# Kernel tuning notes

Measured on AMD Instinct MI355X. Metric: run time of the kernel, lower is better.

## Reference

```python
import jax, jax.numpy as jnp
import numpy as np

B, S, D, H = 4, 2048, 1024, 1024  # batch, seq, input_dim, hidden_dim

def setup_inputs() -> dict:
    key = jax.random.key(0)
    k1, k2, k3, k4, k5 = jax.random.split(key, 5)
    scale1 = 1.0 / np.sqrt(D)
    scale2 = 1.0 / np.sqrt(H)
    return {
        "x": jax.random.normal(k1, (B, S, D), dtype=jnp.float32),
        "W1": jax.random.uniform(k2, (D, 3 * H), jnp.float32, -scale1, scale1),
        "b1": jax.random.uniform(k3, (3 * H,), jnp.float32, -scale1, scale1),
        "W2": jax.random.uniform(k4, (H, H), jnp.float32, -scale2, scale2),
        "b2": jax.random.uniform(k5, (H,), jnp.float32, -scale2, scale2),
    }

def reference(x, W1, b1, W2, b2):
    qkv = jnp.einsum('bsd,dh->bsh', x, W1) + b1          # [B,S,3H]
    q, k, v = jnp.split(qkv, 3, axis=-1)                  # each [B,S,H]
    scale = (2.0 * D) ** -0.5                             # faithful: (input_dim*2)^-0.5
    scores = jnp.einsum('bse,bSe->bsS', q, k) * scale     # [B,S,S]
    att = jax.nn.softmax(scores, axis=-1)
    ctx = jnp.einsum('bsS,bSe->bse', att, v)              # [B,S,H]
    out = jnp.einsum('bsh,hk->bsk', ctx, W2) + b2
    return out
```

## Files before the change

kernel.cpp:

```cpp
#include <hip/hip_runtime.h>
#include <hip/hip_bf16.h>
#include <stdint.h>

#define B_  4
#define S_  2048
#define D_  1024
#define H_  1024
#define BS_ (B_*S_)
#define N3H (3*H_)

typedef __bf16 bf16x8 __attribute__((ext_vector_type(8)));
typedef float  f32x4  __attribute__((ext_vector_type(4)));
typedef unsigned short u16x8 __attribute__((ext_vector_type(8)));

__device__ __forceinline__ unsigned short f2bf(float x) {
    unsigned u = __float_as_uint(x);
    return (unsigned short)((u + 0x7FFFu + ((u >> 16) & 1u)) >> 16);
}
__device__ __forceinline__ float bf2f(unsigned short h) {
    return __uint_as_float(((unsigned)h) << 16);
}

__device__ __forceinline__ void gload_lds16(const void* g, void* l) {
    __builtin_amdgcn_global_load_lds(
        (const __attribute__((address_space(1))) void*)g,
        (__attribute__((address_space(3))) void*)l, 16, 0, 0);
}

#define BAR __builtin_amdgcn_s_barrier()
#define DS_FENCE do { asm volatile("s_waitcnt lgkmcnt(0)" ::: "memory"); \
                      __builtin_amdgcn_sched_barrier(0); } while (0)

template<int EPI>
__global__ __launch_bounds__(256, 3) void gemm3b(
    const unsigned short* __restrict__ A,
    const unsigned short* __restrict__ Bm,
    int NXt, int NYt, int N, int K,
    long long sAz, long long sBz, long long sOz,
    void* __restrict__ out0, void* __restrict__ out1, void* __restrict__ out2,
    const float* __restrict__ bias, float scale)
{
    __shared__ __align__(16) char lds[3 * 16384];

    const int nt_g = (int)gridDim.x;
    const int bid = (int)blockIdx.x;
    const int C = nt_g >> 3;
    const int c = bid >> 3;
    const int xcd = bid & 7;
    const int qq = c >> 2;
    const int txl = qq % NXt;
    const int rest = (c & 3) + 4 * (qq / NXt);
    const int tile = xcd * C + rest * NXt + txl;
    const int tx = tile % NXt;
    const int rest2 = tile / NXt;
    const int ty = rest2 % NYt;
    const int tz = rest2 / NYt;

    const unsigned short* Ab = A  + (long long)tz * sAz;
    const unsigned short* Bb = Bm + (long long)tz * sBz;
    const int rowBase = ty * 128;
    const int colBase = tx * 128;
    const int tid = threadIdx.x;
    const int w = tid >> 6, l = tid & 63;
    const int wr = w >> 1, wc = w & 1;
    const int fr = l & 15, fq = l >> 4;

    int sr[2], scl[2];
#pragma unroll
    for (int j = 0; j < 2; j++) {
        int o  = j * 4096 + tid * 16;
        int st = o >> 10;
        int wi = o & 1023;
        wi ^= ((wi >> 9) & 1) << 5;
        sr[j]  = st * 16 + (wi >> 6);
        scl[j] = (wi & 63) >> 1;
    }

    auto STAGE_A = [&](char* buf, int t) {
        const unsigned short* base = Ab + (long long)rowBase * K + t * 32;
#pragma unroll
        for (int j = 0; j < 2; j++)
            gload_lds16(base + (long long)sr[j] * K + scl[j],
                        buf + j * 4096 + w * 1024);
    };
    auto STAGE_B = [&](char* buf, int t) {
        const unsigned short* base = Bb + (long long)colBase * K + t * 32;
#pragma unroll
        for (int j = 0; j < 2; j++)
            gload_lds16(base + (long long)sr[j] * K + scl[j],
                        buf + 8192 + j * 4096 + w * 1024);
    };

    const int abase = (fr * 64 + fq * 16) ^ ((fr & 8) << 2);

    f32x4 acc[4][4];
#pragma unroll
    for (int m = 0; m < 4; m++)
#pragma unroll
        for (int n = 0; n < 4; n++) acc[m][n] = (f32x4){0.f, 0.f, 0.f, 0.f};

    const int NT = K >> 5;

    STAGE_A(lds, 0); STAGE_B(lds, 0);
    STAGE_A(lds + 16384, 1); STAGE_B(lds + 16384, 1);
    asm volatile("s_waitcnt vmcnt(4)" ::: "memory");
    BAR;
    __builtin_amdgcn_sched_barrier(0);

    bf16x8 af[4], bf[4];

    for (int t = 0; t < NT; ++t) {
        const char* bc = lds + (t % 3) * 16384;
        char* bs = lds + ((t + 2) % 3) * 16384;
        int ts = t + 2; if (ts >= NT) ts -= NT;

#pragma unroll
        for (int m = 0; m < 4; m++)
            af[m] = *(const bf16x8*)(bc + (wr * 4 + m) * 1024 + abase);
#pragma unroll
        for (int n = 0; n < 4; n++)
            bf[n] = *(const bf16x8*)(bc + 8192 + (wc * 4 + n) * 1024 + abase);
        STAGE_A(bs, ts); STAGE_B(bs, ts);
        BAR; DS_FENCE;
        __builtin_amdgcn_s_setprio(1);
#pragma unroll
        for (int m = 0; m < 4; m++)
#pragma unroll
            for (int n = 0; n < 4; n++)
                acc[m][n] = __builtin_amdgcn_mfma_f32_16x16x32_bf16(
                    af[m], bf[n], acc[m][n], 0, 0, 0);
        __builtin_amdgcn_s_setprio(0);
        asm volatile("s_waitcnt vmcnt(4)" ::: "memory");
        BAR;
        __builtin_amdgcn_sched_barrier(0);
    }

    asm volatile("s_waitcnt vmcnt(0) lgkmcnt(0)" ::: "memory");

    const int crow0 = rowBase + wr * 64 + fq * 4;
    const int ccol0 = colBase + wc * 64 + fr;

#pragma unroll
    for (int n = 0; n < 4; n++) {
        const int col = ccol0 + n * 16;
        if constexpr (EPI == 0) {
            const float bv = bias[col];
            const int seg = col >> 10, scn = col & 1023;
            unsigned short* dst =
                (unsigned short*)(seg == 0 ? out0 : (seg == 1 ? out1 : out2));
#pragma unroll
            for (int m = 0; m < 4; m++) {
                const int r0 = crow0 + m * 16;
#pragma unroll
                for (int j = 0; j < 4; j++)
                    dst[(long long)(r0 + j) * 1024 + scn] = f2bf(acc[m][n][j] + bv);
            }
        } else if constexpr (EPI == 1) {
            unsigned short* dst = (unsigned short*)out0 + (long long)tz * sOz;
#pragma unroll
            for (int m = 0; m < 4; m++) {
                const int r0 = crow0 + m * 16;
#pragma unroll
                for (int j = 0; j < 4; j++)
                    dst[(long long)(r0 + j) * N + col] = f2bf(acc[m][n][j] * scale);
            }
        } else {
            float* dst = (float*)out0;
            const float bv = bias[col];
#pragma unroll
            for (int m = 0; m < 4; m++) {
                const int r0 = crow0 + m * 16;
#pragma unroll
                for (int j = 0; j < 4; j++)
                    dst[(long long)(r0 + j) * N + col] = acc[m][n][j] + bv;
            }
        }
    }
}

template<int EPI>
__global__ __launch_bounds__(512, 2) void gemm256(
    const unsigned short* __restrict__ A,
    const unsigned short* __restrict__ Bm,
    int M, int N, int K,
    long long sAz, long long sBz, long long sOz,
    void* __restrict__ out0, void* __restrict__ out1, void* __restrict__ out2,
    const float* __restrict__ bias, float scale)
{
    __shared__ __align__(16) char lds[131072];
    (void)M;

    const unsigned short* Ab = A  + blockIdx.z * sAz;
    const unsigned short* Bb = Bm + blockIdx.z * sBz;
    const int rowBase = blockIdx.y * 256;
    const int colBase = blockIdx.x * 256;
    const int tid = threadIdx.x;
    const int w = tid >> 6, l = tid & 63;
    const int wr = w >> 2, wc = w & 3;
    const int fr = l & 15, fq = l >> 4;

    int sr[2], scl[2];
#pragma unroll
    for (int j = 0; j < 2; j++) {
        int o  = j * 8192 + tid * 16;
        int st = o >> 10;
        int wi = o & 1023;
        wi ^= ((wi >> 9) & 1) << 5;
        sr[j]  = (st >> 1) * 16 + (wi >> 6);
        scl[j] = (st & 1) * 32 + ((wi & 63) >> 1);
    }

    auto STAGE = [&](int buf, int which, int tile) {
        const unsigned short* mat = (which < 2) ? Ab : Bb;
        const int rt0 = ((which < 2) ? rowBase : colBase) + (which & 1) * 128;
        char* dst = lds + buf * 65536 + (which >> 1) * 32768
                        + (which & 1) * 16384 + w * 1024;
        const int k0 = tile * 64;
#pragma unroll
        for (int j = 0; j < 2; j++) {
            const unsigned short* src =
                mat + (long long)(rt0 + sr[j]) * K + k0 + scl[j];
            gload_lds16(src, dst + j * 8192);
        }
    };

    const int abase = (fr * 64 + fq * 16) ^ ((fr & 8) << 2);
    const char* Ah[2] = { lds + wr * 16384, lds + 65536 + wr * 16384 };
    const char* Bh[2] = { lds + 32768 + (wc >> 1) * 16384,
                          lds + 98304 + (wc >> 1) * 16384 };
    const int bn0 = (wc & 1) * 8192;

#define LA(b, m, kk) (*(const bf16x8*)(Ah[b] + (m)*2048 + (kk)*1024 + abase))
#define LB(b, n, kk) (*(const bf16x8*)(Bh[b] + bn0 + (n)*2048 + (kk)*1024 + abase))
#define MFMA16(AF, BF, MOFF, NOFF) do { \
    __builtin_amdgcn_s_setprio(1); \
    _Pragma("unroll") for (int m_ = 0; m_ < 4; m_++) \
    _Pragma("unroll") for (int n_ = 0; n_ < 2; n_++) \
    _Pragma("unroll") for (int k_ = 0; k_ < 2; k_++) \
        acc[(MOFF)+m_][(NOFF)+n_] = __builtin_amdgcn_mfma_f32_16x16x32_bf16( \
            AF[m_][k_], BF[n_][k_], acc[(MOFF)+m_][(NOFF)+n_], 0, 0, 0); \
    __builtin_amdgcn_s_setprio(0); } while (0)

    f32x4 acc[8][4];
#pragma unroll
    for (int m = 0; m < 8; m++)
#pragma unroll
        for (int n = 0; n < 4; n++) acc[m][n] = (f32x4){0.f, 0.f, 0.f, 0.f};

    const int NT = K >> 6;

    STAGE(0, 0, 0); STAGE(0, 1, 0); STAGE(0, 2, 0); STAGE(0, 3, 0);
    STAGE(1, 0, 1); STAGE(1, 1, 1);
    asm volatile("s_waitcnt vmcnt(4)" ::: "memory");
    BAR;
    __builtin_amdgcn_sched_barrier(0);

    bf16x8 afA[4][2], afB[4][2], bfA[2][2], bfB[2][2];

    for (int i = 0; i < NT / 2; i++) {
        const int t1 = 2 * i + 1;
        int t2 = 2 * i + 2; if (t2 >= NT) t2 -= NT;
        int t3 = 2 * i + 3; if (t3 >= NT) t3 -= NT;

#pragma unroll
        for (int m = 0; m < 4; m++) { afA[m][0] = LA(0, m, 0); afA[m][1] = LA(0, m, 1); }
#pragma unroll
        for (int n = 0; n < 2; n++) { bfA[n][0] = LB(0, n, 0); bfA[n][1] = LB(0, n, 1); }
        STAGE(1, 2, t1);
        BAR; DS_FENCE;
        MFMA16(afA, bfA, 0, 0);
        BAR;
#pragma unroll
        for (int m = 0; m < 4; m++) { afB[m][0] = LA(0, 4 + m, 0); afB[m][1] = LA(0, 4 + m, 1); }
        STAGE(1, 3, t1);
        BAR; DS_FENCE;
        MFMA16(afB, bfA, 4, 0);
        BAR;
#pragma unroll
        for (int n = 0; n < 2; n++) { bfB[n][0] = LB(0, 2 + n, 0); bfB[n][1] = LB(0, 2 + n, 1); }
        STAGE(0, 0, t2);
        BAR; DS_FENCE;
        MFMA16(afA, bfB, 0, 2);
        BAR;
        STAGE(0, 1, t2);
        BAR;
        MFMA16(afB, bfB, 4, 2);
        asm volatile("s_waitcnt vmcnt(4)" ::: "memory");
        BAR;
        __builtin_amdgcn_sched_barrier(0);

#pragma unroll
        for (int m = 0; m < 4; m++) { afA[m][0] = LA(1, m, 0); afA[m][1] = LA(1, m, 1); }
#pragma unroll
        for (int n = 0; n < 2; n++) { bfA[n][0] = LB(1, n, 0); bfA[n][1] = LB(1, n, 1); }
        STAGE(0, 2, t2);
        BAR; DS_FENCE;
        MFMA16(afA, bfA, 0, 0);
        BAR;
#pragma unroll
        for (int m = 0; m < 4; m++) { afB[m][0] = LA(1, 4 + m, 0); afB[m][1] = LA(1, 4 + m, 1); }
        STAGE(0, 3, t2);
        BAR; DS_FENCE;
        MFMA16(afB, bfA, 4, 0);
        BAR;
#pragma unroll
        for (int n = 0; n < 2; n++) { bfB[n][0] = LB(1, 2 + n, 0); bfB[n][1] = LB(1, 2 + n, 1); }
        STAGE(1, 0, t3);
        BAR; DS_FENCE;
        MFMA16(afA, bfB, 0, 2);
        BAR;
        STAGE(1, 1, t3);
        BAR;
        MFMA16(afB, bfB, 4, 2);
        asm volatile("s_waitcnt vmcnt(4)" ::: "memory");
        BAR;
        __builtin_amdgcn_sched_barrier(0);
    }

    asm volatile("s_waitcnt vmcnt(0) lgkmcnt(0)" ::: "memory");

    const int crow0 = rowBase + wr * 128 + fq * 4;
    const int ccol0 = colBase + wc * 64 + fr;

#pragma unroll
    for (int n = 0; n < 4; n++) {
        const int col = ccol0 + n * 16;
        if constexpr (EPI == 1) {
            unsigned short* dst = (unsigned short*)out0 + blockIdx.z * sOz;
#pragma unroll
            for (int m = 0; m < 8; m++) {
                const int r0 = crow0 + m * 16;
#pragma unroll
                for (int j = 0; j < 4; j++)
                    dst[(long long)(r0 + j) * N + col] = f2bf(acc[m][n][j] * scale);
            }
        }
    }
    (void)out1; (void)out2; (void)bias;
#undef LA
#undef LB
#undef MFMA16
}

__global__ __launch_bounds__(256) void conv_f32_bf16(
    const float* __restrict__ in, unsigned short* __restrict__ out, int n8)
{
    for (int i = blockIdx.x * blockDim.x + threadIdx.x; i < n8;
         i += gridDim.x * blockDim.x) {
        const float4 a = ((const float4*)in)[2 * i];
        const float4 b = ((const float4*)in)[2 * i + 1];
        u16x8 o;
        o[0] = f2bf(a.x); o[1] = f2bf(a.y); o[2] = f2bf(a.z); o[3] = f2bf(a.w);
        o[4] = f2bf(b.x); o[5] = f2bf(b.y); o[6] = f2bf(b.z); o[7] = f2bf(b.w);
        ((u16x8*)out)[i] = o;
    }
}

__global__ __launch_bounds__(256) void tconv_f32_bf16(
    const float* __restrict__ in, unsigned short* __restrict__ out,
    int rows, int cols)
{
    __shared__ float t[32][33];
    const int c0 = blockIdx.x * 32, r0 = blockIdx.y * 32;
    const int tx = threadIdx.x & 31, ty = threadIdx.x >> 5;
#pragma unroll
    for (int i = 0; i < 4; i++)
        t[ty + 8 * i][tx] = in[(long long)(r0 + ty + 8 * i) * cols + c0 + tx];
    __syncthreads();
#pragma unroll
    for (int i = 0; i < 4; i++)
        out[(long long)(c0 + ty + 8 * i) * rows + r0 + tx] = f2bf(t[tx][ty + 8 * i]);
}

__global__ __launch_bounds__(256) void t_bf16(
    const unsigned short* __restrict__ in, unsigned short* __restrict__ out,
    int rows, int cols, long long sIz, long long sOz)
{
    __shared__ unsigned short t[32][33];
    in  += blockIdx.z * sIz;
    out += blockIdx.z * sOz;
    const int c0 = blockIdx.x * 32, r0 = blockIdx.y * 32;
    const int tx = threadIdx.x & 31, ty = threadIdx.x >> 5;
#pragma unroll
    for (int i = 0; i < 4; i++)
        t[ty + 8 * i][tx] = in[(long long)(r0 + ty + 8 * i) * cols + c0 + tx];
    __syncthreads();
#pragma unroll
    for (int i = 0; i < 4; i++)
        out[(long long)(c0 + ty + 8 * i) * rows + r0 + tx] = t[tx][ty + 8 * i];
}

__global__ __launch_bounds__(256) void softmax_rows(unsigned short* __restrict__ sc)
{
    const long long row = blockIdx.x;
    unsigned short* p = sc + row * S_;
    const int tid = threadIdx.x, w = tid >> 6, l = tid & 63;

    u16x8 v = *reinterpret_cast<const u16x8*>(&p[tid * 8]);
    float f[8];
#pragma unroll
    for (int i = 0; i < 8; i++) f[i] = bf2f(v[i]);

    float m = f[0];
#pragma unroll
    for (int i = 1; i < 8; i++) m = fmaxf(m, f[i]);
    for (int o = 32; o; o >>= 1) m = fmaxf(m, __shfl_xor(m, o));
    __shared__ float red[8];
    if (l == 0) red[w] = m;
    __syncthreads();
    m = fmaxf(fmaxf(red[0], red[1]), fmaxf(red[2], red[3]));

    float s = 0.f;
#pragma unroll
    for (int i = 0; i < 8; i++) { f[i] = __expf(f[i] - m); s += f[i]; }
    for (int o = 32; o; o >>= 1) s += __shfl_xor(s, o);
    if (l == 0) red[4 + w] = s;
    __syncthreads();
    s = red[4] + red[5] + red[6] + red[7];

    const float inv = 1.0f / s;
    u16x8 o8;
#pragma unroll
    for (int i = 0; i < 8; i++) o8[i] = f2bf(f[i] * inv);
    *reinterpret_cast<u16x8*>(&p[tid * 8]) = o8;
}

extern "C" void kernel_launch(void* const* d_in, const int* in_sizes, int n_in,
                              void* d_out, int out_size, void* d_ws, size_t ws_size,
                              hipStream_t stream)
{
    (void)in_sizes; (void)n_in; (void)out_size; (void)ws_size;
    const float* x  = (const float*)d_in[0];
    const float* W1 = (const float*)d_in[1];
    const float* b1 = (const float*)d_in[2];
    const float* W2 = (const float*)d_in[3];
    const float* b2 = (const float*)d_in[4];
    float* out = (float*)d_out;

    char* ws = (char*)d_ws;
    size_t off = 0;
    auto alloc = [&](size_t bytes) {
        void* p = ws + off;
        off += (bytes + 255) & ~(size_t)255;
        return p;
    };
    unsigned short* xbf = (unsigned short*)alloc((size_t)BS_ * D_ * 2);
    unsigned short* w1t = (unsigned short*)alloc((size_t)N3H * D_ * 2);
    unsigned short* w2t = (unsigned short*)alloc((size_t)H_ * H_ * 2);
    unsigned short* q   = (unsigned short*)alloc((size_t)BS_ * H_ * 2);
    unsigned short* k   = (unsigned short*)alloc((size_t)BS_ * H_ * 2);
    unsigned short* v   = (unsigned short*)alloc((size_t)BS_ * H_ * 2);
    unsigned short* vt  = (unsigned short*)alloc((size_t)BS_ * H_ * 2);
    unsigned short* sc  = (unsigned short*)alloc((size_t)B_ * S_ * S_ * 2);
    unsigned short* ctx = v;

    const float scale = 0.022097086912079608f;

    conv_f32_bf16<<<dim3(2048), dim3(256), 0, stream>>>(x, xbf, BS_ * D_ / 8);
    tconv_f32_bf16<<<dim3(N3H / 32, D_ / 32), dim3(256), 0, stream>>>(W1, w1t, D_, N3H);
    tconv_f32_bf16<<<dim3(H_ / 32, H_ / 32), dim3(256), 0, stream>>>(W2, w2t, H_, H_);

    gemm3b<0><<<dim3(1536), dim3(256), 0, stream>>>(
        xbf, w1t, 24, 64, N3H, D_, 0LL, 0LL, 0LL, q, k, v, b1, 1.0f);

    t_bf16<<<dim3(H_ / 32, S_ / 32, B_), dim3(256), 0, stream>>>(
        v, vt, S_, H_, (long long)S_ * H_, (long long)S_ * H_);

    gemm256<1><<<dim3(S_ / 256, S_ / 256, B_), dim3(512), 0, stream>>>(
        q, k, S_, S_, H_, (long long)S_ * H_, (long long)S_ * H_, (long long)S_ * S_,
        sc, nullptr, nullptr, nullptr, scale);

    softmax_rows<<<dim3(BS_), dim3(256), 0, stream>>>(sc);

    gemm3b<1><<<dim3(512), dim3(256), 0, stream>>>(
        sc, vt, 8, 16, H_, S_, (long long)S_ * S_, (long long)H_ * S_,
        (long long)S_ * H_, ctx, nullptr, nullptr, nullptr, 1.0f);

    gemm3b<3><<<dim3(512), dim3(256), 0, stream>>>(
        ctx, w2t, 8, 64, H_, H_, 0LL, 0LL, 0LL, out, nullptr, nullptr, b2, 1.0f);
}
```

Measured before the change: 213.7 us.

## Fuse softmax into QK and PV GEMM epilogues, fuse V transpose into QKV GEMM

Drops the standalone softmax kernel. The QK^T GEMM epilogue now writes exp(scaled score) as bf16 and atomically adds per-row sums into a float buffer. The PV GEMM epilogue divides by those sums. The V transpose is folded into the QKV GEMM epilogue through an LDS staging tile, which removes the separate transpose kernel, and the score GEMM gets an XCD-aware tile remapping. The change skips max subtraction in softmax, relying on small score magnitudes, so it risks overflow for large inputs; it also adds atomics and a memset.

```diff
diff --git a/kernel.cpp b/kernel.cpp
--- a/kernel.cpp
+++ b/kernel.cpp
@@ -136,36 +136,76 @@
     }
 
     asm volatile("s_waitcnt vmcnt(0) lgkmcnt(0)" ::: "memory");
+    BAR;
 
     const int crow0 = rowBase + wr * 64 + fq * 4;
     const int ccol0 = colBase + wc * 64 + fr;
 
-#pragma unroll
-    for (int n = 0; n < 4; n++) {
-        const int col = ccol0 + n * 16;
-        if constexpr (EPI == 0) {
-            const float bv = bias[col];
-            const int seg = col >> 10, scn = col & 1023;
-            unsigned short* dst =
-                (unsigned short*)(seg == 0 ? out0 : (seg == 1 ? out1 : out2));
-#pragma unroll
-            for (int m = 0; m < 4; m++) {
-                const int r0 = crow0 + m * 16;
-#pragma unroll
-                for (int j = 0; j < 4; j++)
-                    dst[(long long)(r0 + j) * 1024 + scn] = f2bf(acc[m][n][j] + bv);
-            }
-        } else if constexpr (EPI == 1) {
-            unsigned short* dst = (unsigned short*)out0 + (long long)tz * sOz;
-#pragma unroll
-            for (int m = 0; m < 4; m++) {
-                const int r0 = crow0 + m * 16;
-#pragma unroll
-                for (int j = 0; j < 4; j++)
-                    dst[(long long)(r0 + j) * N + col] = f2bf(acc[m][n][j] * scale);
+    if constexpr (EPI == 0) {
+        const int seg = colBase >> 10;
+        if (seg < 2) {
+            unsigned short* dst = (unsigned short*)(seg == 0 ? out0 : out1);
+#pragma unroll
+            for (int n = 0; n < 4; n++) {
+                const int col = ccol0 + n * 16;
+                const float bv = bias[col];
+                const int scn = col & 1023;
+#pragma unroll
+                for (int m = 0; m < 4; m++) {
+                    const int r0 = crow0 + m * 16;
+#pragma unroll
+                    for (int j = 0; j < 4; j++)
+                        dst[(long long)(r0 + j) * 1024 + scn] = f2bf(acc[m][n][j] + bv);
+                }
             }
         } else {
-            float* dst = (float*)out0;
+            unsigned short (*T)[129] = (unsigned short(*)[129])lds;
+            const int lr0 = wr * 64 + fq * 4;
+            const int lc0 = wc * 64 + fr;
+#pragma unroll
+            for (int n = 0; n < 4; n++) {
+                const int lc = lc0 + n * 16;
+                const float bv = bias[colBase + lc];
+#pragma unroll
+                for (int m = 0; m < 4; m++)
+#pragma unroll
+                    for (int j = 0; j < 4; j++)
+                        T[lr0 + m * 16 + j][lc] = f2bf(acc[m][n][j] + bv);
+            }
+            BAR;
+            const int s_loc = tid & 127, hh = tid >> 7;
+            const int b = rowBase >> 11;
+            const int s_glob = (rowBase & 2047) + s_loc;
+            unsigned short* vt =
+                (unsigned short*)out2 + (long long)b * ((long long)S_ * H_);
+            const int h0 = (colBase - 2048) + hh * 64;
+#pragma unroll 8
+            for (int h = 0; h < 64; ++h)
+                vt[(long long)(h0 + h) * S_ + s_glob] = T[s_loc][hh * 64 + h];
+        }
+    } else if constexpr (EPI == 4) {
+        unsigned short* dst = (unsigned short*)out0 + (long long)tz * sOz;
+#pragma unroll
+        for (int m = 0; m < 4; m++) {
+            float linv[4];
+#pragma unroll
+            for (int j = 0; j < 4; j++)
+                linv[j] = 1.0f / bias[tz * 2048 + crow0 + m * 16 + j];
+#pragma unroll
+            for (int n = 0; n < 4; n++) {
+                const int col = ccol0 + n * 16;
+                const int r0 = crow0 + m * 16;
+#pragma unroll
+                for (int j = 0; j < 4; j++)
+                    dst[(long long)(r0 + j) * N + col] = f2bf(acc[m][n][j] * linv[j]);
+            }
+        }
+        (void)scale;
+    } else {
+        float* dst = (float*)out0;
+#pragma unroll
+        for (int n = 0; n < 4; n++) {
+            const int col = ccol0 + n * 16;
             const float bv = bias[col];
 #pragma unroll
             for (int m = 0; m < 4; m++) {
@@ -175,6 +215,7 @@
                     dst[(long long)(r0 + j) * N + col] = acc[m][n][j] + bv;
             }
         }
+        (void)scale;
     }
 }
 
@@ -182,18 +223,31 @@
 __global__ __launch_bounds__(512, 2) void gemm256(
     const unsigned short* __restrict__ A,
     const unsigned short* __restrict__ Bm,
-    int M, int N, int K,
+    int NXt, int NYt, int N, int K,
     long long sAz, long long sBz, long long sOz,
     void* __restrict__ out0, void* __restrict__ out1, void* __restrict__ out2,
     const float* __restrict__ bias, float scale)
 {
     __shared__ __align__(16) char lds[131072];
-    (void)M;
-
-    const unsigned short* Ab = A  + blockIdx.z * sAz;
-    const unsigned short* Bb = Bm + blockIdx.z * sBz;
-    const int rowBase = blockIdx.y * 256;
-    const int colBase = blockIdx.x * 256;
+
+    const int nt_g = (int)gridDim.x;
+    const int bid = (int)blockIdx.x;
+    const int C = nt_g >> 3;
+    const int c = bid >> 3;
+    const int xcd = bid & 7;
+    const int qq = c >> 2;
+    const int txl = qq % NXt;
+    const int rest = (c & 3) + 4 * (qq / NXt);
+    const int tile = xcd * C + rest * NXt + txl;
+    const int tx = tile % NXt;
+    const int rest2 = tile / NXt;
+    const int ty = rest2 % NYt;
+    const int tz = rest2 / NYt;
+
+    const unsigned short* Ab = A  + (long long)tz * sAz;
+    const unsigned short* Bb = Bm + (long long)tz * sBz;
+    const int rowBase = ty * 256;
+    const int colBase = tx * 256;
     const int tid = threadIdx.x;
     const int w = tid >> 6, l = tid & 63;
     const int wr = w >> 2, wc = w & 3;
@@ -210,12 +264,12 @@
         scl[j] = (st & 1) * 32 + ((wi & 63) >> 1);
     }
 
-    auto STAGE = [&](int buf, int which, int tile) {
+    auto STAGE = [&](int buf, int which, int tile_) {
         const unsigned short* mat = (which < 2) ? Ab : Bb;
         const int rt0 = ((which < 2) ? rowBase : colBase) + (which & 1) * 128;
         char* dst = lds + buf * 65536 + (which >> 1) * 32768
                         + (which & 1) * 16384 + w * 1024;
-        const int k0 = tile * 64;
+        const int k0 = tile_ * 64;
 #pragma unroll
         for (int j = 0; j < 2; j++) {
             const unsigned short* src =
@@ -322,21 +376,30 @@
     const int crow0 = rowBase + wr * 128 + fq * 4;
     const int ccol0 = colBase + wc * 64 + fr;
 
-#pragma unroll
-    for (int n = 0; n < 4; n++) {
-        const int col = ccol0 + n * 16;
-        if constexpr (EPI == 1) {
-            unsigned short* dst = (unsigned short*)out0 + blockIdx.z * sOz;
-#pragma unroll
-            for (int m = 0; m < 8; m++) {
-                const int r0 = crow0 + m * 16;
-#pragma unroll
-                for (int j = 0; j < 4; j++)
-                    dst[(long long)(r0 + j) * N + col] = f2bf(acc[m][n][j] * scale);
+    if constexpr (EPI == 2) {
+        float* lsum = (float*)out1;
+        unsigned short* dst = (unsigned short*)out0 + (long long)tz * sOz;
+#pragma unroll
+        for (int m = 0; m < 8; m++) {
+#pragma unroll
+            for (int j = 0; j < 4; j++) {
+                const int row = crow0 + m * 16 + j;
+                float rs = 0.f;
+#pragma unroll
+                for (int n = 0; n < 4; n++) {
+                    const int col = ccol0 + n * 16;
+                    const float p = __expf(acc[m][n][j] * scale);
+                    const unsigned short us = f2bf(p);
+                    dst[(long long)row * N + col] = us;
+                    rs += bf2f(us);
+                }
+                rs += __shfl_xor(rs, 1); rs += __shfl_xor(rs, 2);
+                rs += __shfl_xor(rs, 4); rs += __shfl_xor(rs, 8);
+                if (fr == 0) atomicAdd(&lsum[tz * 2048 + row], rs);
             }
         }
     }
-    (void)out1; (void)out2; (void)bias;
+    (void)out2; (void)bias;
 #undef LA
 #undef LB
 #undef MFMA16
@@ -370,59 +433,6 @@
 #pragma unroll
     for (int i = 0; i < 4; i++)
         out[(long long)(c0 + ty + 8 * i) * rows + r0 + tx] = f2bf(t[tx][ty + 8 * i]);
-}
-
-__global__ __launch_bounds__(256) void t_bf16(
-    const unsigned short* __restrict__ in, unsigned short* __restrict__ out,
-    int rows, int cols, long long sIz, long long sOz)
-{
-    __shared__ unsigned short t[32][33];
-    in  += blockIdx.z * sIz;
-    out += blockIdx.z * sOz;
-    const int c0 = blockIdx.x * 32, r0 = blockIdx.y * 32;
-    const int tx = threadIdx.x & 31, ty = threadIdx.x >> 5;
-#pragma unroll
-    for (int i = 0; i < 4; i++)
-        t[ty + 8 * i][tx] = in[(long long)(r0 + ty + 8 * i) * cols + c0 + tx];
-    __syncthreads();
-#pragma unroll
-    for (int i = 0; i < 4; i++)
-        out[(long long)(c0 + ty + 8 * i) * rows + r0 + tx] = t[tx][ty + 8 * i];
-}
-
-__global__ __launch_bounds__(256) void softmax_rows(unsigned short* __restrict__ sc)
-{
-    const long long row = blockIdx.x;
-    unsigned short* p = sc + row * S_;
-    const int tid = threadIdx.x, w = tid >> 6, l = tid & 63;
-
-    u16x8 v = *reinterpret_cast<const u16x8*>(&p[tid * 8]);
-    float f[8];
-#pragma unroll
-    for (int i = 0; i < 8; i++) f[i] = bf2f(v[i]);
-
-    float m = f[0];
-#pragma unroll
-    for (int i = 1; i < 8; i++) m = fmaxf(m, f[i]);
-    for (int o = 32; o; o >>= 1) m = fmaxf(m, __shfl_xor(m, o));
-    __shared__ float red[8];
-    if (l == 0) red[w] = m;
-    __syncthreads();
-    m = fmaxf(fmaxf(red[0], red[1]), fmaxf(red[2], red[3]));
-
-    float s = 0.f;
-#pragma unroll
-    for (int i = 0; i < 8; i++) { f[i] = __expf(f[i] - m); s += f[i]; }
-    for (int o = 32; o; o >>= 1) s += __shfl_xor(s, o);
-    if (l == 0) red[4 + w] = s;
-    __syncthreads();
-    s = red[4] + red[5] + red[6] + red[7];
-
-    const float inv = 1.0f / s;
-    u16x8 o8;
-#pragma unroll
-    for (int i = 0; i < 8; i++) o8[i] = f2bf(f[i] * inv);
-    *reinterpret_cast<u16x8*>(&p[tid * 8]) = o8;
 }
 
 extern "C" void kernel_launch(void* const* d_in, const int* in_sizes, int n_in,
@@ -452,29 +462,27 @@
     unsigned short* v   = (unsigned short*)alloc((size_t)BS_ * H_ * 2);
     unsigned short* vt  = (unsigned short*)alloc((size_t)BS_ * H_ * 2);
     unsigned short* sc  = (unsigned short*)alloc((size_t)B_ * S_ * S_ * 2);
+    float*          lsum = (float*)alloc((size_t)BS_ * 4);
     unsigned short* ctx = v;
 
     const float scale = 0.022097086912079608f;
+
+    hipMemsetAsync(lsum, 0, (size_t)BS_ * 4, stream);
 
     conv_f32_bf16<<<dim3(2048), dim3(256), 0, stream>>>(x, xbf, BS_ * D_ / 8);
     tconv_f32_bf16<<<dim3(N3H / 32, D_ / 32), dim3(256), 0, stream>>>(W1, w1t, D_, N3H);
     tconv_f32_bf16<<<dim3(H_ / 32, H_ / 32), dim3(256), 0, stream>>>(W2, w2t, H_, H_);
 
     gemm3b<0><<<dim3(1536), dim3(256), 0, stream>>>(
-        xbf, w1t, 24, 64, N3H, D_, 0LL, 0LL, 0LL, q, k, v, b1, 1.0f);
-
-    t_bf16<<<dim3(H_ / 32, S_ / 32, B_), dim3(256), 0, stream>>>(
-        v, vt, S_, H_, (long long)S_ * H_, (long long)S_ * H_);
-
-    gemm256<1><<<dim3(S_ / 256, S_ / 256, B_), dim3(512), 0, stream>>>(
-        q, k, S_, S_, H_, (long long)S_ * H_, (long long)S_ * H_, (long long)S_ * S_,
-        sc, nullptr, nullptr, nullptr, scale);
-
-    softmax_rows<<<dim3(BS_), dim3(256), 0, stream>>>(sc);
-
-    gemm3b<1><<<dim3(512), dim3(256), 0, stream>>>(
+        xbf, w1t, 24, 64, N3H, D_, 0LL, 0LL, 0LL, q, k, vt, b1, 1.0f);
+
+    gemm256<2><<<dim3(256), dim3(512), 0, stream>>>(
+        q, k, 8, 8, S_, H_, (long long)S_ * H_, (long long)S_ * H_,
+        (long long)S_ * S_, sc, lsum, nullptr, nullptr, scale);
+
+    gemm3b<4><<<dim3(512), dim3(256), 0, stream>>>(
         sc, vt, 8, 16, H_, S_, (long long)S_ * S_, (long long)H_ * S_,
-        (long long)S_ * H_, ctx, nullptr, nullptr, nullptr, 1.0f);
+        (long long)S_ * H_, ctx, nullptr, nullptr, lsum, 1.0f);
 
     gemm3b<3><<<dim3(512), dim3(256), 0, stream>>>(
         ctx, w2t, 8, 64, H_, H_, 0LL, 0LL, 0LL, out, nullptr, nullptr, b2, 1.0f);
```

Result: faster. 195.6 us (-8.5%).
